# Performance work log

Hardware: AMD Instinct MI355X
Metric: run time of the kernel (lower is better)

## Reference

```python
import jax, jax.numpy as jnp
import numpy as np

N = 8192
IN_F = 256
OUT_F = 64
ALPHA = 0.2
NEG_INF = -9e15


def setup_inputs() -> dict:
    key = jax.random.key(0)
    k1, k2, k3, k4 = jax.random.split(key, 4)
    h = jax.random.normal(k1, (N, IN_F), dtype=jnp.float32)
    W = jax.random.normal(k2, (IN_F, OUT_F), dtype=jnp.float32) * (1.414 / np.sqrt(IN_F))
    a = jax.random.normal(k3, (2 * OUT_F, 1), dtype=jnp.float32) * (1.414 / np.sqrt(2 * OUT_F))
    adj = jax.random.randint(k4, (N, N), 0, 2, dtype=jnp.int32)
    return {"h": h, "W": W, "a": a, "adj": adj}


def reference(h, W, a, adj):
    # Wh: [N, F]
    Wh = h @ W
    # Decompose concat-based attention: e_ij = LeakyReLU(Wh_i . a[:F] + Wh_j . a[F:])
    a1, a2 = a[:OUT_F], a[OUT_F:]
    src = Wh @ a1              # [N, 1] contribution of row i
    dst = Wh @ a2              # [N, 1] contribution of col j
    e = jax.nn.leaky_relu(src + dst.T, negative_slope=ALPHA)  # [N, N]
    e = jnp.where(adj > 0, e, NEG_INF)
    attention = jax.nn.softmax(e, axis=1)
    # dropout is identity in eval mode
    h_prime = attention @ Wh   # [N, F]
    return h_prime
```

## Files before the change

kernel.cpp:

```cpp
#include <hip/hip_runtime.h>

#define NROWS 8192
#define NSPLIT 8
#define JT (NROWS / NSPLIT)
#define NITER (JT / 64)
#define L2E 1.4426950408889634f

typedef __attribute__((ext_vector_type(4))) float f32x4;
typedef __attribute__((ext_vector_type(8))) __bf16 bf16x8;
typedef __attribute__((ext_vector_type(4))) unsigned int u32x4;

__device__ __forceinline__ unsigned short f2bf(float x) {
  unsigned u = __float_as_uint(x);
  u += 0x7fffu + ((u >> 16) & 1u);
  return (unsigned short)(u >> 16);
}

__global__ __launch_bounds__(256) void k_prep(
    const float* __restrict__ h, const float* __restrict__ W,
    const float* __restrict__ a, unsigned short* __restrict__ WhB,
    float* __restrict__ src, float* __restrict__ dst) {
  int i = blockIdx.x * 4 + (threadIdx.x >> 6);
  int lane = threadIdx.x & 63;
  const float* hrow = h + (size_t)i * 256;
  float s = 0.f;
#pragma unroll 4
  for (int k = 0; k < 256; k += 4) {
    float4 hv = *(const float4*)(hrow + k);
    s = fmaf(hv.x, W[(k + 0) * 64 + lane], s);
    s = fmaf(hv.y, W[(k + 1) * 64 + lane], s);
    s = fmaf(hv.z, W[(k + 2) * 64 + lane], s);
    s = fmaf(hv.w, W[(k + 3) * 64 + lane], s);
  }
  int nt = lane >> 4, c = lane & 15;
  int gi = (i >> 3) & 3, e = i & 7;
  int idx = ((((i >> 5) * 4 + nt) * 64) + c + 16 * gi) * 8 + e;
  WhB[idx] = f2bf(s);
  float v1 = s * a[lane];
  float v2 = s * a[64 + lane];
#pragma unroll
  for (int d = 32; d; d >>= 1) {
    v1 += __shfl_xor(v1, d);
    v2 += __shfl_xor(v2, d);
  }
  if (lane == 0) {
    src[i] = v1 * L2E;
    dst[i] = v2 * L2E;
  }
}

__global__ __launch_bounds__(256) void k_dmax(
    const float* __restrict__ dst, float* __restrict__ dmax) {
  __shared__ float red[4];
  float v = -INFINITY;
  for (int i = threadIdx.x; i < NROWS; i += 256) v = fmaxf(v, dst[i]);
#pragma unroll
  for (int d = 32; d; d >>= 1) v = fmaxf(v, __shfl_xor(v, d));
  if ((threadIdx.x & 63) == 0) red[threadIdx.x >> 6] = v;
  __syncthreads();
  if (threadIdx.x == 0)
    *dmax = fmaxf(fmaxf(red[0], red[1]), fmaxf(red[2], red[3]));
}

__global__ __launch_bounds__(256, 4) void k_attn(
    const int* __restrict__ adj, const unsigned short* __restrict__ WhB,
    const float* __restrict__ src, const float* __restrict__ dst,
    const float* __restrict__ dmax,
    float* __restrict__ pl, float* __restrict__ pacc) {
  __shared__ float ldst[JT];
  int task = blockIdx.x * 4 + (threadIdx.x >> 6);
  int sp = task >> 9;
  int mt = task & 511;
  int lane = threadIdx.x & 63;
  int r = lane & 15;
  int g = lane >> 4;
  int row0 = mt * 16;
  int jbase = sp * JT;

  for (int k = threadIdx.x; k < JT; k += 256) ldst[k] = dst[jbase + k];
  __syncthreads();

  unsigned long long mk0 = 0, mk1 = 0, mk2 = 0, mk3 = 0;
  {
    const int* abase = adj + (size_t)row0 * NROWS + jbase + lane;
#pragma unroll
    for (int rr = 0; rr < 16; ++rr) {
      const int* rp = abase + (size_t)rr * NROWS;
#pragma unroll
      for (int ch = 0; ch < 16; ++ch) {
        int v = rp[ch * 64];
        unsigned long long bal = __ballot(v > 0);
        const int holder = ((ch & 3) << 4) + rr;
        if ((ch >> 2) == 0) mk0 = (lane == holder) ? bal : mk0;
        if ((ch >> 2) == 1) mk1 = (lane == holder) ? bal : mk1;
        if ((ch >> 2) == 2) mk2 = (lane == holder) ? bal : mk2;
        if ((ch >> 2) == 3) mk3 = (lane == holder) ? bal : mk3;
      }
    }
  }

  float srcr = src[row0 + r];
  float vB = srcr + *dmax;
  float Mi = fmaxf(vB, 0.2f * vB);

  float lrA = 0.f, lrB = 0.f;
  f32x4 acc[4] = {f32x4{0.f, 0.f, 0.f, 0.f}, f32x4{0.f, 0.f, 0.f, 0.f},
                  f32x4{0.f, 0.f, 0.f, 0.f}, f32x4{0.f, 0.f, 0.f, 0.f}};
  const bf16x8* Bfr = (const bf16x8*)WhB;
  const int jc0 = jbase >> 5;

#define HALF(B0, B1, B2, B3, BITS, DOFF)                                   \
  {                                                                        \
    const float4* dlp = (const float4*)(ldst + (DOFF));                    \
    float4 dA = dlp[0];                                                    \
    float4 dB = dlp[1];                                                    \
    unsigned bt_ = (BITS);                                                 \
    float p0, p1, p2, p3, p4, p5, p6, p7;                                  \
    PE(p0, bt_ & 1u, dA.x)   PE(p1, bt_ & 2u, dA.y)                        \
    PE(p2, bt_ & 4u, dA.z)   PE(p3, bt_ & 8u, dA.w)                        \
    PE(p4, bt_ & 16u, dB.x)  PE(p5, bt_ & 32u, dB.y)                       \
    PE(p6, bt_ & 64u, dB.z)  PE(p7, bt_ & 128u, dB.w)                      \
    lrA += (p0 + p1) + (p2 + p3);                                          \
    lrB += (p4 + p5) + (p6 + p7);                                          \
    unsigned q0, q1, q2, q3;                                               \
    asm("v_cvt_pk_bf16_f32 %0, %1, %2" : "=v"(q0) : "v"(p0), "v"(p1));     \
    asm("v_cvt_pk_bf16_f32 %0, %1, %2" : "=v"(q1) : "v"(p2), "v"(p3));     \
    asm("v_cvt_pk_bf16_f32 %0, %1, %2" : "=v"(q2) : "v"(p4), "v"(p5));     \
    asm("v_cvt_pk_bf16_f32 %0, %1, %2" : "=v"(q3) : "v"(p6), "v"(p7));     \
    u32x4 qv = {q0, q1, q2, q3};                                           \
    bf16x8 Af = __builtin_bit_cast(bf16x8, qv);                            \
    __builtin_amdgcn_s_setprio(1);                                         \
    acc[0] = __builtin_amdgcn_mfma_f32_16x16x32_bf16(Af, B0, acc[0], 0, 0, 0); \
    acc[1] = __builtin_amdgcn_mfma_f32_16x16x32_bf16(Af, B1, acc[1], 0, 0, 0); \
    acc[2] = __builtin_amdgcn_mfma_f32_16x16x32_bf16(Af, B2, acc[2], 0, 0, 0); \
    acc[3] = __builtin_amdgcn_mfma_f32_16x16x32_bf16(Af, B3, acc[3], 0, 0, 0); \
    __builtin_amdgcn_s_setprio(0);                                         \
  }
#define PE(P, BIT, DD)                    \
  {                                       \
    float v_ = srcr + (DD);               \
    v_ = fmaxf(v_, 0.2f * v_);            \
    float e_ = exp2f(v_ - Mi);            \
    (P) = (BIT) ? e_ : 0.f;               \
  }

  const bf16x8* bpA = Bfr + (size_t)jc0 * 256 + lane;
  bf16x8 a0 = bpA[0], a1 = bpA[64], a2 = bpA[128], a3 = bpA[192];

#pragma unroll 1
  for (int it = 0; it < NITER; ++it) {
    int sel = it >> 2;
    unsigned long long msrc = (sel == 0) ? mk0
                            : (sel == 1) ? mk1
                            : (sel == 2) ? mk2 : mk3;
    unsigned long long pw = __shfl(msrc, ((it & 3) << 4) + r);

    const bf16x8* bpB = Bfr + (size_t)(jc0 + 2 * it + 1) * 256 + lane;
    bf16x8 c0 = bpB[0], c1 = bpB[64], c2 = bpB[128], c3 = bpB[192];
    __builtin_amdgcn_sched_barrier(0);

    HALF(a0, a1, a2, a3, (unsigned)(pw >> (8 * g)), it * 64 + 8 * g)

    int jn = (it == NITER - 1) ? jc0 : jc0 + 2 * it + 2;
    const bf16x8* bpN = Bfr + (size_t)jn * 256 + lane;
    a0 = bpN[0]; a1 = bpN[64]; a2 = bpN[128]; a3 = bpN[192];
    __builtin_amdgcn_sched_barrier(0);

    HALF(c0, c1, c2, c3, (unsigned)(pw >> (32 + 8 * g)), it * 64 + 32 + 8 * g)
  }
#undef PE
#undef HALF

  float lrow = lrA + lrB;
  lrow += __shfl_xor(lrow, 16);
  lrow += __shfl_xor(lrow, 32);
  if (lane < 16) pl[sp * NROWS + row0 + lane] = lrow;
#pragma unroll
  for (int nt = 0; nt < 4; nt++)
#pragma unroll
    for (int q2 = 0; q2 < 4; q2++)
      pacc[((size_t)sp * NROWS + row0 + 4 * g + q2) * 64 + nt * 16 + r] = acc[nt][q2];
}

__global__ __launch_bounds__(256) void k_comb(
    const float* __restrict__ pl, const float* __restrict__ pacc,
    float* __restrict__ out) {
  int t = blockIdx.x * 256 + threadIdx.x;
  int row = t >> 6, f = t & 63;
  float L = 0.f, o = 0.f;
#pragma unroll
  for (int s2 = 0; s2 < NSPLIT; s2++) {
    L += pl[s2 * NROWS + row];
    o += pacc[((size_t)s2 * NROWS + row) * 64 + f];
  }
  out[t] = o / L;
}

extern "C" void kernel_launch(void* const* d_in, const int* in_sizes, int n_in,
                              void* d_out, int out_size, void* d_ws, size_t ws_size,
                              hipStream_t stream) {
  const float* h = (const float*)d_in[0];
  const float* W = (const float*)d_in[1];
  const float* a = (const float*)d_in[2];
  const int* adj = (const int*)d_in[3];
  float* out = (float*)d_out;

  char* ws = (char*)d_ws;
  unsigned short* WhB = (unsigned short*)ws;
  float* src = (float*)(ws + 0x100000);
  float* dst = (float*)(ws + 0x108000);
  float* dmax = (float*)(ws + 0x110000);
  float* pl = (float*)(ws + 0x110100);
  float* pacc = (float*)(ws + 0x150100);

  hipLaunchKernelGGL(k_prep, dim3(NROWS / 4), dim3(256), 0, stream, h, W, a, WhB, src, dst);
  hipLaunchKernelGGL(k_dmax, dim3(1), dim3(256), 0, stream, dst, dmax);
  hipLaunchKernelGGL(k_attn, dim3(512 * NSPLIT / 4), dim3(256), 0, stream,
                     adj, WhB, src, dst, dmax, pl, pacc);
  hipLaunchKernelGGL(k_comb, dim3(NROWS * 64 / 256), dim3(256), 0, stream, pl, pacc, out);
}
```

Baseline: 118.8 us.

## Split attention columns 16 ways, raise occupancy, drop register B-prefetch

Doubles the number of column splits so each wave handles 512 columns, with half the adjacency mask registers and half the loop iterations. The launch bound goes to 8 blocks per CU to increase occupancy. The manual double-buffered prefetch of WhB fragments is replaced by direct loads inside each half-step, relying on the extra waves to hide latency. In exchange, the partial accumulator buffer written and re-read by the combine kernel doubles in size, and the workspace offset is moved to fit it.

Result: slower. 132.8 us (+11.8%).

```diff
diff --git a/kernel.cpp b/kernel.cpp
--- a/kernel.cpp
+++ b/kernel.cpp
@@ -1,7 +1,7 @@
 #include <hip/hip_runtime.h>
 
 #define NROWS 8192
-#define NSPLIT 8
+#define NSPLIT 16
 #define JT (NROWS / NSPLIT)
 #define NITER (JT / 64)
 #define L2E 1.4426950408889634f
@@ -62,7 +62,7 @@
     *dmax = fmaxf(fmaxf(red[0], red[1]), fmaxf(red[2], red[3]));
 }
 
-__global__ __launch_bounds__(256, 4) void k_attn(
+__global__ __launch_bounds__(256, 8) void k_attn(
     const int* __restrict__ adj, const unsigned short* __restrict__ WhB,
     const float* __restrict__ src, const float* __restrict__ dst,
     const float* __restrict__ dmax,
@@ -80,21 +80,19 @@
   for (int k = threadIdx.x; k < JT; k += 256) ldst[k] = dst[jbase + k];
   __syncthreads();
 
-  unsigned long long mk0 = 0, mk1 = 0, mk2 = 0, mk3 = 0;
+  unsigned long long mk0 = 0, mk1 = 0;
   {
     const int* abase = adj + (size_t)row0 * NROWS + jbase + lane;
 #pragma unroll
     for (int rr = 0; rr < 16; ++rr) {
       const int* rp = abase + (size_t)rr * NROWS;
 #pragma unroll
-      for (int ch = 0; ch < 16; ++ch) {
+      for (int ch = 0; ch < 8; ++ch) {
         int v = rp[ch * 64];
         unsigned long long bal = __ballot(v > 0);
         const int holder = ((ch & 3) << 4) + rr;
-        if ((ch >> 2) == 0) mk0 = (lane == holder) ? bal : mk0;
-        if ((ch >> 2) == 1) mk1 = (lane == holder) ? bal : mk1;
-        if ((ch >> 2) == 2) mk2 = (lane == holder) ? bal : mk2;
-        if ((ch >> 2) == 3) mk3 = (lane == holder) ? bal : mk3;
+        if (ch < 4) mk0 = (lane == holder) ? bal : mk0;
+        else        mk1 = (lane == holder) ? bal : mk1;
       }
     }
   }
@@ -103,14 +101,25 @@
   float vB = srcr + *dmax;
   float Mi = fmaxf(vB, 0.2f * vB);
 
-  float lrA = 0.f, lrB = 0.f;
+  float lrow = 0.f;
   f32x4 acc[4] = {f32x4{0.f, 0.f, 0.f, 0.f}, f32x4{0.f, 0.f, 0.f, 0.f},
                   f32x4{0.f, 0.f, 0.f, 0.f}, f32x4{0.f, 0.f, 0.f, 0.f}};
   const bf16x8* Bfr = (const bf16x8*)WhB;
-  const int jc0 = jbase >> 5;
-
-#define HALF(B0, B1, B2, B3, BITS, DOFF)                                   \
+
+#define PE(P, BIT, DD)                    \
+  {                                       \
+    float v_ = srcr + (DD);               \
+    v_ = fmaxf(v_, 0.2f * v_);            \
+    float e_ = exp2f(v_ - Mi);            \
+    (P) = (BIT) ? e_ : 0.f;               \
+  }
+#define HALF(JC, BITS, DOFF)                                               \
   {                                                                        \
+    const bf16x8* bp = Bfr + (size_t)(JC) * 256 + lane;                    \
+    bf16x8 b0 = bp[0];                                                     \
+    bf16x8 b1 = bp[64];                                                    \
+    bf16x8 b2 = bp[128];                                                   \
+    bf16x8 b3 = bp[192];                                                   \
     const float4* dlp = (const float4*)(ldst + (DOFF));                    \
     float4 dA = dlp[0];                                                    \
     float4 dB = dlp[1];                                                    \
@@ -120,8 +129,7 @@
     PE(p2, bt_ & 4u, dA.z)   PE(p3, bt_ & 8u, dA.w)                        \
     PE(p4, bt_ & 16u, dB.x)  PE(p5, bt_ & 32u, dB.y)                       \
     PE(p6, bt_ & 64u, dB.z)  PE(p7, bt_ & 128u, dB.w)                      \
-    lrA += (p0 + p1) + (p2 + p3);                                          \
-    lrB += (p4 + p5) + (p6 + p7);                                          \
+    lrow += ((p0 + p1) + (p2 + p3)) + ((p4 + p5) + (p6 + p7));             \
     unsigned q0, q1, q2, q3;                                               \
     asm("v_cvt_pk_bf16_f32 %0, %1, %2" : "=v"(q0) : "v"(p0), "v"(p1));     \
     asm("v_cvt_pk_bf16_f32 %0, %1, %2" : "=v"(q1) : "v"(p2), "v"(p3));     \
@@ -130,48 +138,24 @@
     u32x4 qv = {q0, q1, q2, q3};                                           \
     bf16x8 Af = __builtin_bit_cast(bf16x8, qv);                            \
     __builtin_amdgcn_s_setprio(1);                                         \
-    acc[0] = __builtin_amdgcn_mfma_f32_16x16x32_bf16(Af, B0, acc[0], 0, 0, 0); \
-    acc[1] = __builtin_amdgcn_mfma_f32_16x16x32_bf16(Af, B1, acc[1], 0, 0, 0); \
-    acc[2] = __builtin_amdgcn_mfma_f32_16x16x32_bf16(Af, B2, acc[2], 0, 0, 0); \
-    acc[3] = __builtin_amdgcn_mfma_f32_16x16x32_bf16(Af, B3, acc[3], 0, 0, 0); \
+    acc[0] = __builtin_amdgcn_mfma_f32_16x16x32_bf16(Af, b0, acc[0], 0, 0, 0); \
+    acc[1] = __builtin_amdgcn_mfma_f32_16x16x32_bf16(Af, b1, acc[1], 0, 0, 0); \
+    acc[2] = __builtin_amdgcn_mfma_f32_16x16x32_bf16(Af, b2, acc[2], 0, 0, 0); \
+    acc[3] = __builtin_amdgcn_mfma_f32_16x16x32_bf16(Af, b3, acc[3], 0, 0, 0); \
     __builtin_amdgcn_s_setprio(0);                                         \
   }
-#define PE(P, BIT, DD)                    \
-  {                                       \
-    float v_ = srcr + (DD);               \
-    v_ = fmaxf(v_, 0.2f * v_);            \
-    float e_ = exp2f(v_ - Mi);            \
-    (P) = (BIT) ? e_ : 0.f;               \
-  }
-
-  const bf16x8* bpA = Bfr + (size_t)jc0 * 256 + lane;
-  bf16x8 a0 = bpA[0], a1 = bpA[64], a2 = bpA[128], a3 = bpA[192];
 
 #pragma unroll 1
   for (int it = 0; it < NITER; ++it) {
-    int sel = it >> 2;
-    unsigned long long msrc = (sel == 0) ? mk0
-                            : (sel == 1) ? mk1
-                            : (sel == 2) ? mk2 : mk3;
+    unsigned long long msrc = (it < 4) ? mk0 : mk1;
     unsigned long long pw = __shfl(msrc, ((it & 3) << 4) + r);
-
-    const bf16x8* bpB = Bfr + (size_t)(jc0 + 2 * it + 1) * 256 + lane;
-    bf16x8 c0 = bpB[0], c1 = bpB[64], c2 = bpB[128], c3 = bpB[192];
-    __builtin_amdgcn_sched_barrier(0);
-
-    HALF(a0, a1, a2, a3, (unsigned)(pw >> (8 * g)), it * 64 + 8 * g)
-
-    int jn = (it == NITER - 1) ? jc0 : jc0 + 2 * it + 2;
-    const bf16x8* bpN = Bfr + (size_t)jn * 256 + lane;
-    a0 = bpN[0]; a1 = bpN[64]; a2 = bpN[128]; a3 = bpN[192];
-    __builtin_amdgcn_sched_barrier(0);
-
-    HALF(c0, c1, c2, c3, (unsigned)(pw >> (32 + 8 * g)), it * 64 + 32 + 8 * g)
-  }
+    int jc = sp * 16 + 2 * it;
+    HALF(jc, (unsigned)(pw >> (8 * g)), it * 64 + 8 * g)
+    HALF(jc + 1, (unsigned)(pw >> (32 + 8 * g)), it * 64 + 32 + 8 * g)
+  }
+#undef HALF
 #undef PE
-#undef HALF
-
-  float lrow = lrA + lrB;
+
   lrow += __shfl_xor(lrow, 16);
   lrow += __shfl_xor(lrow, 32);
   if (lane < 16) pl[sp * NROWS + row0 + lane] = lrow;
@@ -211,11 +195,11 @@
   float* dst = (float*)(ws + 0x108000);
   float* dmax = (float*)(ws + 0x110000);
   float* pl = (float*)(ws + 0x110100);
-  float* pacc = (float*)(ws + 0x150100);
+  float* pacc = (float*)(ws + 0x190100);
 
   hipLaunchKernelGGL(k_prep, dim3(NROWS / 4), dim3(256), 0, stream, h, W, a, WhB, src, dst);
   hipLaunchKernelGGL(k_dmax, dim3(1), dim3(256), 0, stream, dst, dmax);
-  hipLaunchKernelGGL(k_attn, dim3(512 * NSPLIT / 4), dim3(256), 0, stream,
+  hipLaunchKernelGGL(k_attn, dim3(2048), dim3(256), 0, stream,
                      adj, WhB, src, dst, dmax, pl, pacc);
   hipLaunchKernelGGL(k_comb, dim3(NROWS * 64 / 256), dim3(256), 0, stream, pl, pacc, out);
 }
```
